# Kernel optimization log

Hardware: AMD Instinct MI355X
Metric: run time of the kernel (lower is better)

Reference implementation:

```python
import jax, jax.numpy as jnp
import numpy as np

N_NODES = 100000
N_EDGES = 1600000
HIDDEN = 64


def setup_inputs() -> dict:
    key = jax.random.key(0)
    k1, k2, k3, k4 = jax.random.split(key, 4)
    x = jax.random.normal(k1, (N_NODES, HIDDEN), dtype=jnp.float32)
    A_rows = jax.random.randint(k2, (N_EDGES,), 0, N_NODES, dtype=jnp.int32)
    A_cols = jax.random.randint(k3, (N_EDGES,), 0, N_NODES, dtype=jnp.int32)
    A_vals = jax.random.uniform(k4, (N_EDGES,), dtype=jnp.float32)
    t = jnp.zeros((), dtype=jnp.float32)
    return {"t": t, "x": x, "A_rows": A_rows, "A_cols": A_cols, "A_vals": A_vals}


def reference(t, x, A_rows, A_cols, A_vals):
    # f = A @ x  (sparse COO SpMM): gather source features, scale, scatter-add to rows
    msgs = A_vals[:, None] * x[A_cols]           # [E, H]
    f = jax.ops.segment_sum(msgs, A_rows, num_segments=N_NODES)  # [N, H]
    # dropout rate is 0.0 -> identity; then ReLU
    return jax.nn.relu(f)
```

## Files before the change

kernel.cpp:

```cpp
#include <hip/hip_runtime.h>
#include <hip/hip_fp16.h>

#define N_NODES 100000
#define N_EDGES 1600000
#define HIDDEN 64
#define RPB 256
#define NCB ((N_NODES + RPB - 1) / RPB)
#define CAP 4608
#define R1_THREADS 512
#define R1_BATCH 6144
#define R1_PER_T (R1_BATCH / R1_THREADS)
#define SORT_SLOTS ((CAP + 1023) / 1024)

__global__ void __launch_bounds__(256) conv_fp16_zero_kernel(const float4* __restrict__ x4,
                                                             ushort4* __restrict__ xh,
                                                             int* __restrict__ ccursor,
                                                             int n4) {
    if (blockIdx.x == 0)
        for (int i = threadIdx.x; i < NCB; i += 256) ccursor[i] = 0;
    int i = blockIdx.x * blockDim.x + threadIdx.x;
    const int stride = gridDim.x * blockDim.x;
    for (; i < n4; i += stride) {
        const float4 v = x4[i];
        ushort4 q;
        q.x = __half_as_ushort(__float2half(v.x));
        q.y = __half_as_ushort(__float2half(v.y));
        q.z = __half_as_ushort(__float2half(v.z));
        q.w = __half_as_ushort(__float2half(v.w));
        xh[i] = q;
    }
}

__global__ void __launch_bounds__(R1_THREADS) coarse_scatter_pad_kernel(
        const int* __restrict__ rows, const int* __restrict__ cols,
        const float* __restrict__ vals, int* __restrict__ ccursor,
        int2* __restrict__ cbuf) {
    __shared__ int hist[NCB];
    __shared__ int base[NCB];
    const int t = threadIdx.x;
    const int b0 = blockIdx.x * R1_BATCH;
    for (int i = t; i < NCB; i += R1_THREADS) hist[i] = 0;
    __syncthreads();

    int  mb[R1_PER_T];
    int  rk[R1_PER_T];
    int2 md[R1_PER_T];
    #pragma unroll
    for (int k = 0; k < R1_PER_T; ++k) {
        const int e = b0 + k * R1_THREADS + t;
        mb[k] = -1;
        if (e < N_EDGES) {
            const int r = rows[e];
            mb[k] = r >> 8;
            md[k] = make_int2(((r & (RPB - 1)) << 17) | cols[e], __float_as_int(vals[e]));
            rk[k] = atomicAdd(&hist[mb[k]], 1);
        }
    }
    __syncthreads();
    for (int i = t; i < NCB; i += R1_THREADS) {
        const int c = hist[i];
        base[i] = c ? (i * CAP + atomicAdd(&ccursor[i], c)) : 0;
    }
    __syncthreads();
    #pragma unroll
    for (int k = 0; k < R1_PER_T; ++k)
        if (mb[k] >= 0) cbuf[base[mb[k]] + rk[k]] = md[k];
}

__global__ void __launch_bounds__(1024) sort_spmm_kernel(
        const int2* __restrict__ cbuf, const int* __restrict__ ccursor,
        const ushort4* __restrict__ xh, float4* __restrict__ out4) {
    __shared__ int s[2][RPB];
    __shared__ int rowstart[RPB + 1];
    __shared__ int2 se[CAP + 16];
    const int b = blockIdx.x;
    const int t = threadIdx.x;
    const int cnt  = min(ccursor[b], CAP);
    const int src0 = b * CAP;

    if (t < RPB) s[0][t] = 0;
    __syncthreads();

    int  rw[SORT_SLOTS];
    int  rk[SORT_SLOTS];
    int2 md[SORT_SLOTS];
    #pragma unroll
    for (int k = 0; k < SORT_SLOTS; ++k) {
        const int i = k * 1024 + t;
        rw[k] = -1;
        if (i < cnt) {
            const int2 m = cbuf[src0 + i];
            const int row = (m.x >> 17) & (RPB - 1);
            rw[k] = row;
            md[k] = make_int2(m.x & 0x1FFFF, m.y);
            rk[k] = atomicAdd(&s[0][row], 1);
        }
    }
    __syncthreads();
    int src = 0;
    for (int off = 1; off < RPB; off <<= 1) {
        if (t < RPB) s[1 - src][t] = s[src][t] + (t >= off ? s[src][t - off] : 0);
        __syncthreads();
        src ^= 1;
    }
    if (t < RPB) rowstart[t] = t ? s[src][t - 1] : 0;
    if (t == 0) rowstart[RPB] = cnt;
    __syncthreads();
    #pragma unroll
    for (int k = 0; k < SORT_SLOTS; ++k)
        if (rw[k] >= 0) se[rowstart[rw[k]] + rk[k]] = md[k];
    __syncthreads();

    const int lane = t & 63;
    const int wave = t >> 6;
    const int g = lane >> 4;
    const int h = lane & 15;
    #pragma unroll 1
    for (int rj = 0; rj < RPB / 16; ++rj) {
        const int row = wave * 16 + rj;
        const int start = rowstart[row], end = rowstart[row + 1];
        float4 acc = make_float4(0.f, 0.f, 0.f, 0.f);
        for (int eb = start; eb < end; eb += 16) {
            const int i0 = eb + g, i1 = eb + 4 + g, i2 = eb + 8 + g, i3 = eb + 12 + g;
            const int2 m0 = se[i0];
            const int2 m1 = se[i1];
            const int2 m2 = se[i2];
            const int2 m3 = se[i3];
            const bool p0 = i0 < end, p1 = i1 < end, p2 = i2 < end, p3 = i3 < end;
            const int   c0 = p0 ? m0.x : 0;
            const float v0 = p0 ? __int_as_float(m0.y) : 0.f;
            const int   c1 = p1 ? m1.x : 0;
            const float v1 = p1 ? __int_as_float(m1.y) : 0.f;
            const int   c2 = p2 ? m2.x : 0;
            const float v2 = p2 ? __int_as_float(m2.y) : 0.f;
            const int   c3 = p3 ? m3.x : 0;
            const float v3 = p3 ? __int_as_float(m3.y) : 0.f;
            const ushort4 q0 = xh[(size_t)c0 * 16 + h];
            const ushort4 q1 = xh[(size_t)c1 * 16 + h];
            const ushort4 q2 = xh[(size_t)c2 * 16 + h];
            const ushort4 q3 = xh[(size_t)c3 * 16 + h];
            acc.x = fmaf(v0, __half2float(__ushort_as_half(q0.x)), acc.x);
            acc.y = fmaf(v0, __half2float(__ushort_as_half(q0.y)), acc.y);
            acc.z = fmaf(v0, __half2float(__ushort_as_half(q0.z)), acc.z);
            acc.w = fmaf(v0, __half2float(__ushort_as_half(q0.w)), acc.w);
            acc.x = fmaf(v1, __half2float(__ushort_as_half(q1.x)), acc.x);
            acc.y = fmaf(v1, __half2float(__ushort_as_half(q1.y)), acc.y);
            acc.z = fmaf(v1, __half2float(__ushort_as_half(q1.z)), acc.z);
            acc.w = fmaf(v1, __half2float(__ushort_as_half(q1.w)), acc.w);
            acc.x = fmaf(v2, __half2float(__ushort_as_half(q2.x)), acc.x);
            acc.y = fmaf(v2, __half2float(__ushort_as_half(q2.y)), acc.y);
            acc.z = fmaf(v2, __half2float(__ushort_as_half(q2.z)), acc.z);
            acc.w = fmaf(v2, __half2float(__ushort_as_half(q2.w)), acc.w);
            acc.x = fmaf(v3, __half2float(__ushort_as_half(q3.x)), acc.x);
            acc.y = fmaf(v3, __half2float(__ushort_as_half(q3.y)), acc.y);
            acc.z = fmaf(v3, __half2float(__ushort_as_half(q3.z)), acc.z);
            acc.w = fmaf(v3, __half2float(__ushort_as_half(q3.w)), acc.w);
        }
        acc.x += __shfl_xor(acc.x, 16); acc.y += __shfl_xor(acc.y, 16);
        acc.z += __shfl_xor(acc.z, 16); acc.w += __shfl_xor(acc.w, 16);
        acc.x += __shfl_xor(acc.x, 32); acc.y += __shfl_xor(acc.y, 32);
        acc.z += __shfl_xor(acc.z, 32); acc.w += __shfl_xor(acc.w, 32);
        const int rg = b * RPB + row;
        if (lane < 16 && rg < N_NODES) {
            float4 o;
            o.x = fmaxf(acc.x, 0.f); o.y = fmaxf(acc.y, 0.f);
            o.z = fmaxf(acc.z, 0.f); o.w = fmaxf(acc.w, 0.f);
            out4[(size_t)rg * 16 + h] = o;
        }
    }
}

__global__ void spmm_scatter_kernel(const float* __restrict__ x,
                                    const int* __restrict__ rows,
                                    const int* __restrict__ cols,
                                    const float* __restrict__ vals,
                                    float* __restrict__ f) {
    const int lane = threadIdx.x & 63;
    const int wave = (blockIdx.x * blockDim.x + threadIdx.x) >> 6;
    const int nWaves = (gridDim.x * blockDim.x) >> 6;
    for (int e = wave; e < N_EDGES; e += nWaves)
        atomicAdd(&f[rows[e] * HIDDEN + lane], vals[e] * x[cols[e] * HIDDEN + lane]);
}
__global__ void relu_inplace_kernel(float4* __restrict__ f, int n4) {
    int i = blockIdx.x * blockDim.x + threadIdx.x;
    const int stride = gridDim.x * blockDim.x;
    for (; i < n4; i += stride) {
        float4 v = f[i];
        v.x = fmaxf(v.x, 0.0f); v.y = fmaxf(v.y, 0.0f);
        v.z = fmaxf(v.z, 0.0f); v.w = fmaxf(v.w, 0.0f);
        f[i] = v;
    }
}

extern "C" void kernel_launch(void* const* d_in, const int* in_sizes, int n_in,
                              void* d_out, int out_size, void* d_ws, size_t ws_size,
                              hipStream_t stream) {
    const float* x    = (const float*)d_in[1];
    const int*   rows = (const int*)d_in[2];
    const int*   cols = (const int*)d_in[3];
    const float* vals = (const float*)d_in[4];
    float* out = (float*)d_out;
    char* ws = (char*)d_ws;

    const size_t ccursor_off = 0;
    size_t cbuf_off = ccursor_off + (size_t)NCB * 4;
    cbuf_off = (cbuf_off + 15) & ~(size_t)15;
    const size_t xh_off  = cbuf_off + (size_t)NCB * CAP * 8;
    const size_t ws_need = xh_off + (size_t)N_NODES * HIDDEN * 2;

    if (ws_size >= ws_need) {
        int*     ccursor = (int*)(ws + ccursor_off);
        int2*    cbuf    = (int2*)(ws + cbuf_off);
        ushort4* xh      = (ushort4*)(ws + xh_off);

        conv_fp16_zero_kernel<<<2048, 256, 0, stream>>>(
            (const float4*)x, xh, ccursor, N_NODES * HIDDEN / 4);
        coarse_scatter_pad_kernel<<<(N_EDGES + R1_BATCH - 1) / R1_BATCH, R1_THREADS,
                                    0, stream>>>(rows, cols, vals, ccursor, cbuf);
        sort_spmm_kernel<<<NCB, 1024, 0, stream>>>(cbuf, ccursor,
                                                   (const ushort4*)xh, (float4*)out);
        return;
    }

    hipMemsetAsync(d_out, 0, (size_t)N_NODES * HIDDEN * sizeof(float), stream);
    spmm_scatter_kernel<<<2048, 256, 0, stream>>>(x, rows, cols, vals, out);
    relu_inplace_kernel<<<2048, 256, 0, stream>>>((float4*)d_out,
                                                  (N_NODES * HIDDEN) / 4);
}
```

Before: 87.82 us.

## Stage coarse bucket scatter through shared memory for coalesced global writes

The coarse binning kernel now prefix-scans the per-bucket histogram, places each edge into a block-local sorted staging array in shared memory, and then writes contiguous runs to each bucket's global slot. The goal is to replace scattered 8-byte global stores with mostly coalesced ones. The batch per block shrinks so the staging array and its auxiliary bucket-id array fit in LDS. The cost is an extra scan, additional barriers and more LDS per block, which may lower occupancy.

```diff
diff --git a/kernel.cpp b/kernel.cpp
--- a/kernel.cpp
+++ b/kernel.cpp
@@ -8,7 +8,7 @@
 #define NCB ((N_NODES + RPB - 1) / RPB)
 #define CAP 4608
 #define R1_THREADS 512
-#define R1_BATCH 6144
+#define R1_BATCH 4096
 #define R1_PER_T (R1_BATCH / R1_THREADS)
 #define SORT_SLOTS ((CAP + 1023) / 1024)
 
@@ -31,12 +31,16 @@
     }
 }
 
-__global__ void __launch_bounds__(R1_THREADS) coarse_scatter_pad_kernel(
+__global__ void __launch_bounds__(R1_THREADS) coarse_stage_kernel(
         const int* __restrict__ rows, const int* __restrict__ cols,
         const float* __restrict__ vals, int* __restrict__ ccursor,
         int2* __restrict__ cbuf) {
     __shared__ int hist[NCB];
-    __shared__ int base[NCB];
+    __shared__ int lstart[NCB + 1];
+    __shared__ int gbase[NCB];
+    __shared__ unsigned short aux[R1_BATCH];
+    __shared__ int2 se[R1_BATCH];
+    __shared__ int sc[2][R1_THREADS];
     const int t = threadIdx.x;
     const int b0 = blockIdx.x * R1_BATCH;
     for (int i = t; i < NCB; i += R1_THREADS) hist[i] = 0;
@@ -57,14 +61,32 @@
         }
     }
     __syncthreads();
+    sc[0][t] = (t < NCB) ? hist[t] : 0;
+    __syncthreads();
+    int src = 0;
+    for (int off = 1; off < R1_THREADS; off <<= 1) {
+        sc[1 - src][t] = sc[src][t] + (t >= off ? sc[src][t - off] : 0);
+        __syncthreads();
+        src ^= 1;
+    }
+    if (t < NCB) lstart[t] = t ? sc[src][t - 1] : 0;
+    if (t == 0) lstart[NCB] = sc[src][NCB - 1];
+    __syncthreads();
     for (int i = t; i < NCB; i += R1_THREADS) {
         const int c = hist[i];
-        base[i] = c ? (i * CAP + atomicAdd(&ccursor[i], c)) : 0;
-    }
-    __syncthreads();
+        gbase[i] = c ? (i * CAP + atomicAdd(&ccursor[i], c)) : 0;
+    }
     #pragma unroll
     for (int k = 0; k < R1_PER_T; ++k)
-        if (mb[k] >= 0) cbuf[base[mb[k]] + rk[k]] = md[k];
+        if (mb[k] >= 0) se[lstart[mb[k]] + rk[k]] = md[k];
+    for (int b = t; b < NCB; b += R1_THREADS)
+        for (int i = lstart[b]; i < lstart[b + 1]; ++i) aux[i] = (unsigned short)b;
+    __syncthreads();
+    const int total = lstart[NCB];
+    for (int i = t; i < total; i += R1_THREADS) {
+        const int b = aux[i];
+        cbuf[gbase[b] + (i - lstart[b])] = se[i];
+    }
 }
 
 __global__ void __launch_bounds__(1024) sort_spmm_kernel(
@@ -215,8 +237,8 @@
 
         conv_fp16_zero_kernel<<<2048, 256, 0, stream>>>(
             (const float4*)x, xh, ccursor, N_NODES * HIDDEN / 4);
-        coarse_scatter_pad_kernel<<<(N_EDGES + R1_BATCH - 1) / R1_BATCH, R1_THREADS,
-                                    0, stream>>>(rows, cols, vals, ccursor, cbuf);
+        coarse_stage_kernel<<<(N_EDGES + R1_BATCH - 1) / R1_BATCH, R1_THREADS,
+                              0, stream>>>(rows, cols, vals, ccursor, cbuf);
         sort_spmm_kernel<<<NCB, 1024, 0, stream>>>(cbuf, ccursor,
                                                    (const ushort4*)xh, (float4*)out);
         return;
```

After: 84.61 us (median of 2 runs). 3.6% less time.
